# Kernel optimization log

Measured on AMD Instinct MI355X. Metric: run time of the kernel, lower is better.

Reference implementation:

```python
import jax, jax.numpy as jnp
import numpy as np

N_NODES = 100000
N_CELLS = 200000
N_EDGES = 300000
D = 128            # input_size == attention_size
HID = 128          # hidden width of custom_func MLP
SCALE = np.sqrt(np.float32(D))


def segment_softmax(src, seg_ids, num_segments):
    # src: [M, 1], seg_ids: [M] -> softmax normalized within each segment
    m = jax.ops.segment_max(src, seg_ids, num_segments=num_segments)
    e = jnp.exp(src - m[seg_ids])
    s = jax.ops.segment_sum(e, seg_ids, num_segments=num_segments)
    return e / s[seg_ids]


def setup_inputs() -> dict:
    key = jax.random.key(0)
    ks = jax.random.split(key, 9)
    cell_attr = jax.random.normal(ks[0], (N_CELLS, D), dtype=jnp.float32)
    edge_attr = jax.random.normal(ks[1], (N_EDGES, D), dtype=jnp.float32)
    node_embedding = jax.random.normal(ks[2], (N_NODES, D), dtype=jnp.float32)
    edge_index = jax.random.randint(ks[3], (2, N_EDGES), 0, N_NODES, dtype=jnp.int32)
    face = jax.random.randint(ks[4], (3, N_CELLS), 0, N_NODES, dtype=jnp.int32)
    # custom_func: 2-layer MLP (2D -> HID -> D)
    W1 = jax.random.normal(ks[5], (2 * D, HID), dtype=jnp.float32) / np.sqrt(2 * D)
    b1 = jnp.zeros((HID,), dtype=jnp.float32)
    W2 = jax.random.normal(ks[6], (HID, D), dtype=jnp.float32) / np.sqrt(HID)
    b2 = jnp.zeros((D,), dtype=jnp.float32)
    return {"cell_attr": cell_attr, "edge_attr": edge_attr,
            "node_embedding": node_embedding, "edge_index": edge_index,
            "face": face, "W1": W1, "b1": b1, "W2": W2, "b2": b2}


def reference(cell_attr, edge_attr, node_embedding, edge_index, face, W1, b1, W2, b2):
    senders, receivers = edge_index[0], edge_index[1]
    two_out = jnp.concatenate([receivers, senders], axis=0)   # outdegree order [2E]
    two_edge = jnp.concatenate([edge_attr, edge_attr], axis=0)  # [2E, D]

    # attention over edges grouped by target (outdegree) node
    att_src = jnp.sum(two_edge * node_embedding[two_out], axis=1, keepdims=True) / SCALE
    att = segment_softmax(att_src, two_out, N_NODES)            # [2E, 1]
    node_agg = jax.ops.segment_sum(two_edge * att, two_out, num_segments=N_NODES)  # [N, D]

    # cells gather mean of their 3 nodes
    cell_agg = (node_agg[face[0]] + node_agg[face[1]] + node_agg[face[2]]) / 3.0  # [C, D]

    # custom_func MLP on cat(cell_attr, cell_agg)
    h = jax.nn.relu(jnp.concatenate([cell_attr, cell_agg], axis=1) @ W1 + b1)
    cell_attr_new = h @ W2 + b2                                  # [C, D]

    # scatter_mean of cell features back to nodes
    cells_node_index = jnp.concatenate([face[0], face[1], face[2]], axis=0)  # [3C]
    tripled = jnp.concatenate([cell_attr_new] * 3, axis=0)                   # [3C, D]
    sums = jax.ops.segment_sum(tripled, cells_node_index, num_segments=N_NODES)
    counts = jax.ops.segment_sum(jnp.ones((3 * N_CELLS,), jnp.float32),
                                 cells_node_index, num_segments=N_NODES)
    node_attr = sums / jnp.maximum(counts, 1.0)[:, None]

    return cell_attr_new, node_attr
```

## Files before the change

kernel.cpp:

```cpp
#include <hip/hip_runtime.h>

#define NN 100000
#define NC 200000
#define NE 300000
#define D  128

typedef unsigned short u16;
typedef __attribute__((ext_vector_type(8))) short bf16x8;
typedef __attribute__((ext_vector_type(4))) float f32x4;

__device__ __forceinline__ u16 f2bf(float x) {
    unsigned int u = __float_as_uint(x);
    u += 0x7fffu + ((u >> 16) & 1u);
    return (u16)(u >> 16);
}
__device__ __forceinline__ float bf2f(u16 h) {
    return __uint_as_float((unsigned int)h << 16);
}

#define MFMA16(a, b, c) __builtin_amdgcn_mfma_f32_16x16x32_bf16((a), (b), (c), 0, 0, 0)

__global__ __launch_bounds__(256) void k_att(const float* __restrict__ edge_attr,
                                             const float* __restrict__ emb,
                                             const int* __restrict__ ei,
                                             float* __restrict__ expv,
                                             float* __restrict__ denom) {
    int e = blockIdx.x * 4 + (threadIdx.x >> 6);
    int lane = threadIdx.x & 63;
    if (e >= NE) return;
    int send = ei[e];
    int recv = ei[NE + e];
    float2 a = ((const float2*)(edge_attr + (size_t)e * D))[lane];
    float2 r = ((const float2*)(emb + (size_t)recv * D))[lane];
    float2 s = ((const float2*)(emb + (size_t)send * D))[lane];
    float dr = a.x * r.x + a.y * r.y;
    float ds = a.x * s.x + a.y * s.y;
    #pragma unroll
    for (int off = 32; off > 0; off >>= 1) {
        dr += __shfl_xor(dr, off);
        ds += __shfl_xor(ds, off);
    }
    if (lane == 0) {
        const float inv_scale = 0.08838834764831845f;
        float er = __expf(dr * inv_scale);
        float es = __expf(ds * inv_scale);
        expv[e] = er;
        expv[NE + e] = es;
        atomicAdd(&denom[recv], er);
        atomicAdd(&denom[send], es);
    }
}

__global__ __launch_bounds__(256) void k_hist_att(const int* __restrict__ ei,
                                                  int* __restrict__ cnt) {
    int i = blockIdx.x * 256 + threadIdx.x;
    if (i >= 2 * NE) return;
    int t = (i < NE) ? ei[NE + i] : ei[i - NE];
    atomicAdd(&cnt[t], 1);
}

__global__ __launch_bounds__(256) void k_hist_face(const int* __restrict__ face,
                                                   int* __restrict__ cnt) {
    int i = blockIdx.x * 256 + threadIdx.x;
    if (i >= 3 * NC) return;
    atomicAdd(&cnt[face[i]], 1);
}

__global__ __launch_bounds__(256) void k_scan_blocks(const int* __restrict__ cnt,
                                                     int* __restrict__ bsum) {
    __shared__ int s[256];
    int t = threadIdx.x;
    int i = blockIdx.x * 256 + t;
    s[t] = (i < NN) ? cnt[i] : 0;
    __syncthreads();
    #pragma unroll
    for (int off = 128; off > 0; off >>= 1) {
        if (t < off) s[t] += s[t + off];
        __syncthreads();
    }
    if (t == 0) bsum[blockIdx.x] = s[0];
}

__global__ __launch_bounds__(512) void k_scan_top(int* __restrict__ bsum, int nb) {
    __shared__ int s[512];
    int t = threadIdx.x;
    int v = (t < nb) ? bsum[t] : 0;
    s[t] = v;
    __syncthreads();
    #pragma unroll
    for (int off = 1; off < 512; off <<= 1) {
        int x = (t >= off) ? s[t - off] : 0;
        __syncthreads();
        s[t] += x;
        __syncthreads();
    }
    if (t < nb) bsum[t] = s[t] - v;
}

__global__ __launch_bounds__(256) void k_scan_final(const int* __restrict__ cnt,
                                                    const int* __restrict__ bsum,
                                                    int* __restrict__ off_out,
                                                    int total) {
    __shared__ int s[256];
    int t = threadIdx.x;
    int i = blockIdx.x * 256 + t;
    int v = (i < NN) ? cnt[i] : 0;
    s[t] = v;
    __syncthreads();
    #pragma unroll
    for (int off = 1; off < 256; off <<= 1) {
        int x = (t >= off) ? s[t - off] : 0;
        __syncthreads();
        s[t] += x;
        __syncthreads();
    }
    if (i < NN) off_out[i] = s[t] - v + bsum[blockIdx.x];
    if (i == 0) off_out[NN] = total;
}

__global__ __launch_bounds__(256) void k_fill_att(const int* __restrict__ ei,
                                                  const int* __restrict__ offs,
                                                  int* __restrict__ cur,
                                                  int* __restrict__ slots) {
    int i = blockIdx.x * 256 + threadIdx.x;
    if (i >= 2 * NE) return;
    int t = (i < NE) ? ei[NE + i] : ei[i - NE];
    int pos = offs[t] + atomicAdd(&cur[t], 1);
    slots[pos] = i;
}

__global__ __launch_bounds__(256) void k_fill_face(const int* __restrict__ face,
                                                   const int* __restrict__ offs,
                                                   int* __restrict__ cur,
                                                   int* __restrict__ slots) {
    int i = blockIdx.x * 256 + threadIdx.x;
    if (i >= 3 * NC) return;
    int t = face[i];
    int pos = offs[t] + atomicAdd(&cur[t], 1);
    int c = i; if (c >= NC) c -= NC; if (c >= NC) c -= NC;
    slots[pos] = c;
}

__global__ __launch_bounds__(256) void k_agg_gather(const float* __restrict__ edge_attr,
                                                    const float* __restrict__ expv,
                                                    const float* __restrict__ denom,
                                                    const int* __restrict__ offs,
                                                    const int* __restrict__ slots,
                                                    float* __restrict__ na) {
    int n = blockIdx.x * 4 + (threadIdx.x >> 6);
    int lane = threadIdx.x & 63;
    if (n >= NN) return;
    int s0 = offs[n], s1 = offs[n + 1];
    float2 acc = {0.f, 0.f};
    for (int s = s0; s < s1; ++s) {
        int eid = slots[s];
        int row = (eid < NE) ? eid : eid - NE;
        float w = expv[eid];
        float2 a = ((const float2*)(edge_attr + (size_t)row * D))[lane];
        acc.x += w * a.x;
        acc.y += w * a.y;
    }
    float inv = (s1 > s0) ? 1.f / denom[n] : 0.f;
    float2* p = (float2*)(na + (size_t)n * D) + lane;
    float2 r; r.x = acc.x * inv; r.y = acc.y * inv;
    *p = r;
}

__global__ __launch_bounds__(256) void k_smean_gather(const float* __restrict__ cell_out,
                                                      const int* __restrict__ offs,
                                                      const int* __restrict__ slots,
                                                      float* __restrict__ node_out) {
    int n = blockIdx.x * 4 + (threadIdx.x >> 6);
    int lane = threadIdx.x & 63;
    if (n >= NN) return;
    int s0 = offs[n], s1 = offs[n + 1];
    float2 acc = {0.f, 0.f};
    for (int s = s0; s < s1; ++s) {
        int c = slots[s];
        float2 y = ((const float2*)(cell_out + (size_t)c * D))[lane];
        acc.x += y.x;
        acc.y += y.y;
    }
    int deg = s1 - s0;
    float inv = deg ? 1.f / (float)deg : 0.f;
    float2* p = (float2*)(node_out + (size_t)n * D) + lane;
    float2 r; r.x = acc.x * inv; r.y = acc.y * inv;
    *p = r;
}

__global__ __launch_bounds__(256) void k_wsplit(const float* __restrict__ W1,
                                                const float* __restrict__ W2,
                                                u16* __restrict__ w1h, u16* __restrict__ w1l,
                                                u16* __restrict__ w2h, u16* __restrict__ w2l) {
    int tid = blockIdx.x * 256 + threadIdx.x;
    if (tid >= 6144) return;
    int l = tid & 63;
    int f = tid >> 6;
    const float* W; u16 *oh, *ol; int fi;
    if (f < 64) { W = W1; oh = w1h; ol = w1l; fi = f; }
    else        { W = W2; oh = w2h; ol = w2l; fi = f - 64; }
    int kt = fi >> 3, nt = fi & 7;
    int k0 = kt * 32 + 8 * (l >> 4);
    int n  = nt * 16 + (l & 15);
    #pragma unroll
    for (int i = 0; i < 8; i++) {
        float x = W[(size_t)(k0 + i) * 128 + n];
        u16 h = f2bf(x);
        oh[(size_t)fi * 512 + l * 8 + i] = h;
        ol[(size_t)fi * 512 + l * 8 + i] = f2bf(x - bf2f(h));
    }
}

__device__ __forceinline__ void stage_split(char* lds, int row, int col8, const float* v) {
    unsigned int byte = ((unsigned int)row << 9) + ((unsigned int)col8 << 4);
    byte ^= (unsigned int)(row & 7) << 4;
    bf16x8 hi, lo;
    #pragma unroll
    for (int i = 0; i < 8; i++) {
        u16 h = f2bf(v[i]);
        hi[i] = (short)h;
        lo[i] = (short)f2bf(v[i] - bf2f(h));
    }
    *(bf16x8*)(lds + byte)         = hi;
    *(bf16x8*)(lds + 16384 + byte) = lo;
}

__global__ __launch_bounds__(256, 4) void k_mlp(const float* __restrict__ cell_attr,
                                                const float* __restrict__ na,
                                                const int* __restrict__ face,
                                                const u16* __restrict__ w1h,
                                                const u16* __restrict__ w1l,
                                                const u16* __restrict__ w2h,
                                                const u16* __restrict__ w2l,
                                                const float* __restrict__ b1,
                                                const float* __restrict__ b2,
                                                float* __restrict__ out) {
    __shared__ char lds[32768];
    const int t  = threadIdx.x;
    const int c0 = blockIdx.x * 32;

    {
        const int r = t >> 3;
        const int q = t & 7;
        float v[16];
        const float* pa = cell_attr + (size_t)(c0 + r) * D + q * 16;
        #pragma unroll
        for (int i = 0; i < 4; i++) *(float4*)(v + 4 * i) = *(const float4*)(pa + 4 * i);
        stage_split(lds, r, q * 2,     v);
        stage_split(lds, r, q * 2 + 1, v + 8);

        const int cid = c0 + r;
        const int f0 = face[cid], f1 = face[NC + cid], f2 = face[2 * NC + cid];
        const float* p0 = na + (size_t)f0 * D + q * 16;
        const float* p1 = na + (size_t)f1 * D + q * 16;
        const float* p2 = na + (size_t)f2 * D + q * 16;
        const float third = 1.f / 3.f;
        #pragma unroll
        for (int i = 0; i < 4; i++) {
            float4 a0 = *(const float4*)(p0 + 4 * i);
            float4 a1 = *(const float4*)(p1 + 4 * i);
            float4 a2 = *(const float4*)(p2 + 4 * i);
            v[4 * i + 0] = (a0.x + a1.x + a2.x) * third;
            v[4 * i + 1] = (a0.y + a1.y + a2.y) * third;
            v[4 * i + 2] = (a0.z + a1.z + a2.z) * third;
            v[4 * i + 3] = (a0.w + a1.w + a2.w) * third;
        }
        stage_split(lds, r, 16 + q * 2, v);
        stage_split(lds, r, 17 + q * 2, v + 8);
    }
    __syncthreads();

    const int w  = t >> 6;
    const int l  = t & 63;
    const int lr = l & 15;
    const int lg = l >> 4;
    const unsigned int swz = (unsigned int)(lr & 7) << 4;
    const size_t wl8 = (size_t)l * 8;
    const f32x4 z4 = {0.f, 0.f, 0.f, 0.f};
    f32x4 acc[2][2] = {{z4, z4}, {z4, z4}};

    {
        const unsigned int abase = ((unsigned int)lr << 9) + ((unsigned int)lg << 4);
        const u16* pW1h = w1h + (size_t)(w * 2) * 512 + wl8;
        const u16* pW1l = w1l + (size_t)(w * 2) * 512 + wl8;
        #pragma unroll 2
        for (int kt = 0; kt < 8; ++kt) {
            unsigned int ab = (abase + (unsigned int)kt * 64) ^ swz;
            bf16x8 aH0 = *(const bf16x8*)(lds + ab);
            bf16x8 aL0 = *(const bf16x8*)(lds + 16384 + ab);
            bf16x8 aH1 = *(const bf16x8*)(lds + ab + 8192);
            bf16x8 aL1 = *(const bf16x8*)(lds + 16384 + ab + 8192);
            #pragma unroll
            for (int jn = 0; jn < 2; ++jn) {
                size_t fo = (size_t)(kt * 8 + jn) * 512;
                bf16x8 bH = *(const bf16x8*)(pW1h + fo);
                bf16x8 bL = *(const bf16x8*)(pW1l + fo);
                acc[0][jn] = MFMA16(aH0, bL, acc[0][jn]);
                acc[0][jn] = MFMA16(aL0, bH, acc[0][jn]);
                acc[0][jn] = MFMA16(aH0, bH, acc[0][jn]);
                acc[1][jn] = MFMA16(aH1, bL, acc[1][jn]);
                acc[1][jn] = MFMA16(aL1, bH, acc[1][jn]);
                acc[1][jn] = MFMA16(aH1, bH, acc[1][jn]);
            }
        }
    }

    __syncthreads();

    #pragma unroll
    for (int jn = 0; jn < 2; ++jn) {
        int col = w * 32 + jn * 16 + lr;
        float bb = b1[col];
        #pragma unroll
        for (int rt = 0; rt < 2; ++rt) {
            #pragma unroll
            for (int r = 0; r < 4; ++r) {
                int row = rt * 16 + lg * 4 + r;
                float h = fmaxf(acc[rt][jn][r] + bb, 0.f);
                u16 hh = f2bf(h);
                u16 hl = f2bf(h - bf2f(hh));
                unsigned int byte = (((unsigned int)row << 8) + ((unsigned int)col << 1))
                                    ^ ((unsigned int)(row & 7) << 4);
                *(u16*)(lds + byte)        = hh;
                *(u16*)(lds + 8192 + byte) = hl;
            }
        }
    }
    __syncthreads();

    f32x4 acc2[2][2] = {{z4, z4}, {z4, z4}};
    {
        const unsigned int abase = ((unsigned int)lr << 8) + ((unsigned int)lg << 4);
        const u16* pW2h = w2h + (size_t)(w * 2) * 512 + wl8;
        const u16* pW2l = w2l + (size_t)(w * 2) * 512 + wl8;
        #pragma unroll 2
        for (int kt = 0; kt < 4; ++kt) {
            unsigned int ab = (abase + (unsigned int)kt * 64) ^ swz;
            bf16x8 aH0 = *(const bf16x8*)(lds + ab);
            bf16x8 aL0 = *(const bf16x8*)(lds + 8192 + ab);
            bf16x8 aH1 = *(const bf16x8*)(lds + ab + 4096);
            bf16x8 aL1 = *(const bf16x8*)(lds + 8192 + ab + 4096);
            #pragma unroll
            for (int jn = 0; jn < 2; ++jn) {
                size_t fo = (size_t)(kt * 8 + jn) * 512;
                bf16x8 bH = *(const bf16x8*)(pW2h + fo);
                bf16x8 bL = *(const bf16x8*)(pW2l + fo);
                acc2[0][jn] = MFMA16(aH0, bL, acc2[0][jn]);
                acc2[0][jn] = MFMA16(aL0, bH, acc2[0][jn]);
                acc2[0][jn] = MFMA16(aH0, bH, acc2[0][jn]);
                acc2[1][jn] = MFMA16(aH1, bL, acc2[1][jn]);
                acc2[1][jn] = MFMA16(aL1, bH, acc2[1][jn]);
                acc2[1][jn] = MFMA16(aH1, bH, acc2[1][jn]);
            }
        }
    }

    #pragma unroll
    for (int jn = 0; jn < 2; ++jn) {
        int col = w * 32 + jn * 16 + lr;
        float bb = b2[col];
        #pragma unroll
        for (int rt = 0; rt < 2; ++rt) {
            #pragma unroll
            for (int r = 0; r < 4; ++r) {
                int row = c0 + rt * 16 + lg * 4 + r;
                out[(size_t)row * D + col] = acc2[rt][jn][r] + bb;
            }
        }
    }
}

extern "C" void kernel_launch(void* const* d_in, const int* in_sizes, int n_in,
                              void* d_out, int out_size, void* d_ws, size_t ws_size,
                              hipStream_t stream) {
    (void)in_sizes; (void)n_in; (void)out_size; (void)ws_size;
    const float* cell_attr = (const float*)d_in[0];
    const float* edge_attr = (const float*)d_in[1];
    const float* emb       = (const float*)d_in[2];
    const int*   ei        = (const int*)d_in[3];
    const int*   face      = (const int*)d_in[4];
    const float* W1        = (const float*)d_in[5];
    const float* b1        = (const float*)d_in[6];
    const float* W2        = (const float*)d_in[7];
    const float* b2        = (const float*)d_in[8];

    float* out_cell = (float*)d_out;
    float* out_node = out_cell + (size_t)NC * D;

    float* denom  = (float*)d_ws;
    int*   cntA   = (int*)d_ws + NN;
    int*   cntF   = cntA + NN;
    int*   curA   = cntF + NN;
    int*   curF   = curA + NN;
    float* expv   = (float*)(curF + NN);
    int*   offA   = (int*)(expv + 2 * NE);
    int*   offF   = offA + NN + 1;
    int*   slotsA = offF + NN + 1;
    int*   slotsF = slotsA + 2 * NE;
    int*   bsumA  = slotsF + 3 * NC;
    int*   bsumF  = bsumA + 512;

    u16* w1h = (u16*)curA;
    u16* w1l = w1h + 64 * 512;
    u16* w2h = w1l + 64 * 512;
    u16* w2l = w2h + 32 * 512;

    const int NB = (NN + 255) / 256;

    hipMemsetAsync(d_ws, 0, (size_t)5 * NN * 4, stream);

    k_att<<<(NE + 3) / 4, 256, 0, stream>>>(edge_attr, emb, ei, expv, denom);

    k_hist_att <<<(2 * NE + 255) / 256, 256, 0, stream>>>(ei, cntA);
    k_hist_face<<<(3 * NC + 255) / 256, 256, 0, stream>>>(face, cntF);

    k_scan_blocks<<<NB, 256, 0, stream>>>(cntA, bsumA);
    k_scan_top   <<<1, 512, 0, stream>>>(bsumA, NB);
    k_scan_final <<<NB, 256, 0, stream>>>(cntA, bsumA, offA, 2 * NE);

    k_scan_blocks<<<NB, 256, 0, stream>>>(cntF, bsumF);
    k_scan_top   <<<1, 512, 0, stream>>>(bsumF, NB);
    k_scan_final <<<NB, 256, 0, stream>>>(cntF, bsumF, offF, 3 * NC);

    k_fill_att <<<(2 * NE + 255) / 256, 256, 0, stream>>>(ei, offA, curA, slotsA);
    k_fill_face<<<(3 * NC + 255) / 256, 256, 0, stream>>>(face, offF, curF, slotsF);

    k_wsplit<<<24, 256, 0, stream>>>(W1, W2, w1h, w1l, w2h, w2l);

    k_agg_gather<<<(NN + 3) / 4, 256, 0, stream>>>(edge_attr, expv, denom, offA, slotsA, out_node);

    k_mlp<<<NC / 32, 256, 0, stream>>>(cell_attr, out_node, face,
                                       w1h, w1l, w2h, w2l, b1, b2, out_cell);

    k_smean_gather<<<(NN + 3) / 4, 256, 0, stream>>>(out_cell, offF, slotsF, out_node);
}
```

Before: 748.4 us.

## Fuse prep kernels, pre-resolve slot weights, and widen gathers to float4

Merges the attention, histogram, and weight-split kernels into one launch, and batches the two scans and two fill passes into shared launches, cutting the launch count. The fill pass now stores the edge row and its exp weight per slot, so the aggregation no longer does an indirect expv lookup. Both gather kernels switch to float4 loads with two half-waves each taking alternate neighbours, then combine with a shuffle. BF16 hi/lo splitting uses the packed v_cvt_pk_bf16_f32 instruction. Weight-split buffers move to a separate workspace region, because they previously overlapped the cur counters that now run alongside them.

```diff
diff --git a/kernel.cpp b/kernel.cpp
--- a/kernel.cpp
+++ b/kernel.cpp
@@ -4,6 +4,9 @@
 #define NC 200000
 #define NE 300000
 #define D  128
+#define NB 391
+#define AB 37500
+#define HB 2344
 
 typedef unsigned short u16;
 typedef __attribute__((ext_vector_type(8))) short bf16x8;
@@ -17,60 +20,96 @@
 __device__ __forceinline__ float bf2f(u16 h) {
     return __uint_as_float((unsigned int)h << 16);
 }
+__device__ __forceinline__ unsigned int cvt_pk_bf16(float a, float b) {
+    unsigned int r;
+    asm("v_cvt_pk_bf16_f32 %0, %1, %2" : "=v"(r) : "v"(a), "v"(b));
+    return r;
+}
 
 #define MFMA16(a, b, c) __builtin_amdgcn_mfma_f32_16x16x32_bf16((a), (b), (c), 0, 0, 0)
 
-__global__ __launch_bounds__(256) void k_att(const float* __restrict__ edge_attr,
-                                             const float* __restrict__ emb,
-                                             const int* __restrict__ ei,
-                                             float* __restrict__ expv,
-                                             float* __restrict__ denom) {
-    int e = blockIdx.x * 4 + (threadIdx.x >> 6);
-    int lane = threadIdx.x & 63;
-    if (e >= NE) return;
-    int send = ei[e];
-    int recv = ei[NE + e];
-    float2 a = ((const float2*)(edge_attr + (size_t)e * D))[lane];
-    float2 r = ((const float2*)(emb + (size_t)recv * D))[lane];
-    float2 s = ((const float2*)(emb + (size_t)send * D))[lane];
-    float dr = a.x * r.x + a.y * r.y;
-    float ds = a.x * s.x + a.y * s.y;
-    #pragma unroll
-    for (int off = 32; off > 0; off >>= 1) {
-        dr += __shfl_xor(dr, off);
-        ds += __shfl_xor(ds, off);
-    }
-    if (lane == 0) {
-        const float inv_scale = 0.08838834764831845f;
-        float er = __expf(dr * inv_scale);
-        float es = __expf(ds * inv_scale);
-        expv[e] = er;
-        expv[NE + e] = es;
-        atomicAdd(&denom[recv], er);
-        atomicAdd(&denom[send], es);
-    }
-}
-
-__global__ __launch_bounds__(256) void k_hist_att(const int* __restrict__ ei,
-                                                  int* __restrict__ cnt) {
-    int i = blockIdx.x * 256 + threadIdx.x;
-    if (i >= 2 * NE) return;
-    int t = (i < NE) ? ei[NE + i] : ei[i - NE];
-    atomicAdd(&cnt[t], 1);
-}
-
-__global__ __launch_bounds__(256) void k_hist_face(const int* __restrict__ face,
-                                                   int* __restrict__ cnt) {
-    int i = blockIdx.x * 256 + threadIdx.x;
-    if (i >= 3 * NC) return;
-    atomicAdd(&cnt[face[i]], 1);
-}
-
-__global__ __launch_bounds__(256) void k_scan_blocks(const int* __restrict__ cnt,
-                                                     int* __restrict__ bsum) {
+__global__ __launch_bounds__(256) void k_att_prep(const float* __restrict__ edge_attr,
+                                                  const float* __restrict__ emb,
+                                                  const int* __restrict__ ei,
+                                                  const int* __restrict__ face,
+                                                  float* __restrict__ expv,
+                                                  float* __restrict__ denom,
+                                                  int* __restrict__ cntA,
+                                                  int* __restrict__ cntF,
+                                                  const float* __restrict__ W1,
+                                                  const float* __restrict__ W2,
+                                                  u16* __restrict__ w1h, u16* __restrict__ w1l,
+                                                  u16* __restrict__ w2h, u16* __restrict__ w2l) {
+    int b = blockIdx.x;
+    int t = threadIdx.x;
+    if (b < AB) {
+        int lane = t & 63;
+        int half = lane >> 5;
+        int sub  = lane & 31;
+        int e = b * 8 + (t >> 6) * 2 + half;
+        int send = ei[e];
+        int recv = ei[NE + e];
+        float4 a  = ((const float4*)(edge_attr + (size_t)e * D))[sub];
+        float4 r4 = ((const float4*)(emb + (size_t)recv * D))[sub];
+        float4 s4 = ((const float4*)(emb + (size_t)send * D))[sub];
+        float dr = a.x * r4.x + a.y * r4.y + a.z * r4.z + a.w * r4.w;
+        float ds = a.x * s4.x + a.y * s4.y + a.z * s4.z + a.w * s4.w;
+        #pragma unroll
+        for (int off = 16; off > 0; off >>= 1) {
+            dr += __shfl_xor(dr, off);
+            ds += __shfl_xor(ds, off);
+        }
+        if (sub == 0) {
+            const float inv_scale = 0.08838834764831845f;
+            float er = __expf(dr * inv_scale);
+            float es = __expf(ds * inv_scale);
+            expv[e] = er;
+            expv[NE + e] = es;
+            atomicAdd(&denom[recv], er);
+            atomicAdd(&denom[send], es);
+        }
+    } else if (b < AB + HB) {
+        int i = (b - AB) * 256 + t;
+        if (i >= 2 * NE) return;
+        int tgt = (i < NE) ? ei[NE + i] : ei[i - NE];
+        atomicAdd(&cntA[tgt], 1);
+    } else if (b < AB + 2 * HB) {
+        int i = (b - AB - HB) * 256 + t;
+        if (i >= 3 * NC) return;
+        atomicAdd(&cntF[face[i]], 1);
+    } else {
+        int tid = (b - AB - 2 * HB) * 256 + t;
+        if (tid >= 6144) return;
+        int l = tid & 63;
+        int f = tid >> 6;
+        const float* W; u16 *oh, *ol; int fi;
+        if (f < 64) { W = W1; oh = w1h; ol = w1l; fi = f; }
+        else        { W = W2; oh = w2h; ol = w2l; fi = f - 64; }
+        int kt = fi >> 3, nt = fi & 7;
+        int k0 = kt * 32 + 8 * (l >> 4);
+        int n  = nt * 16 + (l & 15);
+        #pragma unroll
+        for (int i = 0; i < 8; i++) {
+            float x = W[(size_t)(k0 + i) * 128 + n];
+            u16 h = f2bf(x);
+            oh[(size_t)fi * 512 + l * 8 + i] = h;
+            ol[(size_t)fi * 512 + l * 8 + i] = f2bf(x - bf2f(h));
+        }
+    }
+}
+
+__global__ __launch_bounds__(256) void k_scan_blocks(const int* __restrict__ cntA,
+                                                     const int* __restrict__ cntF,
+                                                     int* __restrict__ bsumA,
+                                                     int* __restrict__ bsumF) {
     __shared__ int s[256];
+    int bb = blockIdx.x;
+    bool fa = bb >= NB;
+    const int* cnt = fa ? cntF : cntA;
+    int* bsum = fa ? bsumF : bsumA;
+    int blk = fa ? bb - NB : bb;
     int t = threadIdx.x;
-    int i = blockIdx.x * 256 + t;
+    int i = blk * 256 + t;
     s[t] = (i < NN) ? cnt[i] : 0;
     __syncthreads();
     #pragma unroll
@@ -78,11 +117,13 @@
         if (t < off) s[t] += s[t + off];
         __syncthreads();
     }
-    if (t == 0) bsum[blockIdx.x] = s[0];
-}
-
-__global__ __launch_bounds__(512) void k_scan_top(int* __restrict__ bsum, int nb) {
+    if (t == 0) bsum[blk] = s[0];
+}
+
+__global__ __launch_bounds__(512) void k_scan_top(int* __restrict__ bsumA,
+                                                  int* __restrict__ bsumF, int nb) {
     __shared__ int s[512];
+    int* bsum = blockIdx.x ? bsumF : bsumA;
     int t = threadIdx.x;
     int v = (t < nb) ? bsum[t] : 0;
     s[t] = v;
@@ -97,13 +138,22 @@
     if (t < nb) bsum[t] = s[t] - v;
 }
 
-__global__ __launch_bounds__(256) void k_scan_final(const int* __restrict__ cnt,
-                                                    const int* __restrict__ bsum,
-                                                    int* __restrict__ off_out,
-                                                    int total) {
+__global__ __launch_bounds__(256) void k_scan_final(const int* __restrict__ cntA,
+                                                    const int* __restrict__ cntF,
+                                                    const int* __restrict__ bsumA,
+                                                    const int* __restrict__ bsumF,
+                                                    int* __restrict__ offA,
+                                                    int* __restrict__ offF) {
     __shared__ int s[256];
+    int bb = blockIdx.x;
+    bool fa = bb >= NB;
+    const int* cnt = fa ? cntF : cntA;
+    const int* bsum = fa ? bsumF : bsumA;
+    int* off_out = fa ? offF : offA;
+    int total = fa ? 3 * NC : 2 * NE;
+    int blk = fa ? bb - NB : bb;
     int t = threadIdx.x;
-    int i = blockIdx.x * 256 + t;
+    int i = blk * 256 + t;
     int v = (i < NN) ? cnt[i] : 0;
     s[t] = v;
     __syncthreads();
@@ -114,56 +164,66 @@
         s[t] += x;
         __syncthreads();
     }
-    if (i < NN) off_out[i] = s[t] - v + bsum[blockIdx.x];
+    if (i < NN) off_out[i] = s[t] - v + bsum[blk];
     if (i == 0) off_out[NN] = total;
 }
 
-__global__ __launch_bounds__(256) void k_fill_att(const int* __restrict__ ei,
-                                                  const int* __restrict__ offs,
-                                                  int* __restrict__ cur,
-                                                  int* __restrict__ slots) {
-    int i = blockIdx.x * 256 + threadIdx.x;
-    if (i >= 2 * NE) return;
-    int t = (i < NE) ? ei[NE + i] : ei[i - NE];
-    int pos = offs[t] + atomicAdd(&cur[t], 1);
-    slots[pos] = i;
-}
-
-__global__ __launch_bounds__(256) void k_fill_face(const int* __restrict__ face,
-                                                   const int* __restrict__ offs,
-                                                   int* __restrict__ cur,
-                                                   int* __restrict__ slots) {
-    int i = blockIdx.x * 256 + threadIdx.x;
-    if (i >= 3 * NC) return;
-    int t = face[i];
-    int pos = offs[t] + atomicAdd(&cur[t], 1);
-    int c = i; if (c >= NC) c -= NC; if (c >= NC) c -= NC;
-    slots[pos] = c;
+__global__ __launch_bounds__(256) void k_fill(const int* __restrict__ ei,
+                                              const float* __restrict__ expv,
+                                              const int* __restrict__ face,
+                                              const int* __restrict__ offA,
+                                              const int* __restrict__ offF,
+                                              int* __restrict__ curA,
+                                              int* __restrict__ curF,
+                                              int* __restrict__ slotsA,
+                                              float* __restrict__ wexpA,
+                                              int* __restrict__ slotsF) {
+    int b = blockIdx.x;
+    int t = threadIdx.x;
+    if (b < HB) {
+        int i = b * 256 + t;
+        if (i >= 2 * NE) return;
+        int tgt = (i < NE) ? ei[NE + i] : ei[i - NE];
+        int pos = offA[tgt] + atomicAdd(&curA[tgt], 1);
+        slotsA[pos] = (i < NE) ? i : i - NE;
+        wexpA[pos] = expv[i];
+    } else {
+        int i = (b - HB) * 256 + t;
+        if (i >= 3 * NC) return;
+        int tgt = face[i];
+        int pos = offF[tgt] + atomicAdd(&curF[tgt], 1);
+        int c = i; if (c >= NC) c -= NC; if (c >= NC) c -= NC;
+        slotsF[pos] = c;
+    }
 }
 
 __global__ __launch_bounds__(256) void k_agg_gather(const float* __restrict__ edge_attr,
-                                                    const float* __restrict__ expv,
+                                                    const float* __restrict__ wexp,
                                                     const float* __restrict__ denom,
                                                     const int* __restrict__ offs,
                                                     const int* __restrict__ slots,
                                                     float* __restrict__ na) {
     int n = blockIdx.x * 4 + (threadIdx.x >> 6);
     int lane = threadIdx.x & 63;
+    int half = lane >> 5, sub = lane & 31;
     if (n >= NN) return;
     int s0 = offs[n], s1 = offs[n + 1];
-    float2 acc = {0.f, 0.f};
-    for (int s = s0; s < s1; ++s) {
-        int eid = slots[s];
-        int row = (eid < NE) ? eid : eid - NE;
-        float w = expv[eid];
-        float2 a = ((const float2*)(edge_attr + (size_t)row * D))[lane];
-        acc.x += w * a.x;
-        acc.y += w * a.y;
-    }
-    float inv = (s1 > s0) ? 1.f / denom[n] : 0.f;
-    float2* p = (float2*)(na + (size_t)n * D) + lane;
-    float2 r; r.x = acc.x * inv; r.y = acc.y * inv;
-    *p = r;
+    float4 acc = {0.f, 0.f, 0.f, 0.f};
+    for (int s = s0 + half; s < s1; s += 2) {
+        int row = slots[s];
+        float w = wexp[s];
+        float4 a = ((const float4*)(edge_attr + (size_t)row * D))[sub];
+        acc.x += w * a.x; acc.y += w * a.y; acc.z += w * a.z; acc.w += w * a.w;
+    }
+    acc.x += __shfl_xor(acc.x, 32);
+    acc.y += __shfl_xor(acc.y, 32);
+    acc.z += __shfl_xor(acc.z, 32);
+    acc.w += __shfl_xor(acc.w, 32);
+    if (half == 0) {
+        float inv = (s1 > s0) ? 1.f / denom[n] : 0.f;
+        float4 r; r.x = acc.x * inv; r.y = acc.y * inv; r.z = acc.z * inv; r.w = acc.w * inv;
+        ((float4*)(na + (size_t)n * D))[sub] = r;
+    }
 }
 
 __global__ __launch_bounds__(256) void k_smean_gather(const float* __restrict__ cell_out,
@@ -172,57 +232,43 @@
                                                       float* __restrict__ node_out) {
     int n = blockIdx.x * 4 + (threadIdx.x >> 6);
     int lane = threadIdx.x & 63;
+    int half = lane >> 5, sub = lane & 31;
     if (n >= NN) return;
     int s0 = offs[n], s1 = offs[n + 1];
-    float2 acc = {0.f, 0.f};
-    for (int s = s0; s < s1; ++s) {
+    float4 acc = {0.f, 0.f, 0.f, 0.f};
+    for (int s = s0 + half; s < s1; s += 2) {
         int c = slots[s];
-        float2 y = ((const float2*)(cell_out + (size_t)c * D))[lane];
-        acc.x += y.x;
-        acc.y += y.y;
-    }
-    int deg = s1 - s0;
-    float inv = deg ? 1.f / (float)deg : 0.f;
-    float2* p = (float2*)(node_out + (size_t)n * D) + lane;
-    float2 r; r.x = acc.x * inv; r.y = acc.y * inv;
-    *p = r;
-}
-
-__global__ __launch_bounds__(256) void k_wsplit(const float* __restrict__ W1,
-                                                const float* __restrict__ W2,
-                                                u16* __restrict__ w1h, u16* __restrict__ w1l,
-                                                u16* __restrict__ w2h, u16* __restrict__ w2l) {
-    int tid = blockIdx.x * 256 + threadIdx.x;
-    if (tid >= 6144) return;
-    int l = tid & 63;
-    int f = tid >> 6;
-    const float* W; u16 *oh, *ol; int fi;
-    if (f < 64) { W = W1; oh = w1h; ol = w1l; fi = f; }
-    else        { W = W2; oh = w2h; ol = w2l; fi = f - 64; }
-    int kt = fi >> 3, nt = fi & 7;
-    int k0 = kt * 32 + 8 * (l >> 4);
-    int n  = nt * 16 + (l & 15);
-    #pragma unroll
-    for (int i = 0; i < 8; i++) {
-        float x = W[(size_t)(k0 + i) * 128 + n];
-        u16 h = f2bf(x);
-        oh[(size_t)fi * 512 + l * 8 + i] = h;
-        ol[(size_t)fi * 512 + l * 8 + i] = f2bf(x - bf2f(h));
+        float4 y = ((const float4*)(cell_out + (size_t)c * D))[sub];
+        acc.x += y.x; acc.y += y.y; acc.z += y.z; acc.w += y.w;
+    }
+    acc.x += __shfl_xor(acc.x, 32);
+    acc.y += __shfl_xor(acc.y, 32);
+    acc.z += __shfl_xor(acc.z, 32);
+    acc.w += __shfl_xor(acc.w, 32);
+    if (half == 0) {
+        int deg = s1 - s0;
+        float inv = deg ? 1.f / (float)deg : 0.f;
+        float4 r; r.x = acc.x * inv; r.y = acc.y * inv; r.z = acc.z * inv; r.w = acc.w * inv;
+        ((float4*)(node_out + (size_t)n * D))[sub] = r;
     }
 }
 
 __device__ __forceinline__ void stage_split(char* lds, int row, int col8, const float* v) {
     unsigned int byte = ((unsigned int)row << 9) + ((unsigned int)col8 << 4);
     byte ^= (unsigned int)(row & 7) << 4;
-    bf16x8 hi, lo;
+    uint4 hi, lo;
+    unsigned int* hp = (unsigned int*)&hi;
+    unsigned int* lp = (unsigned int*)&lo;
     #pragma unroll
-    for (int i = 0; i < 8; i++) {
-        u16 h = f2bf(v[i]);
-        hi[i] = (short)h;
-        lo[i] = (short)f2bf(v[i] - bf2f(h));
-    }
-    *(bf16x8*)(lds + byte)         = hi;
-    *(bf16x8*)(lds + 16384 + byte) = lo;
+    for (int i = 0; i < 4; i++) {
+        unsigned int h = cvt_pk_bf16(v[2 * i], v[2 * i + 1]);
+        float h0 = __uint_as_float(h << 16);
+        float h1 = __uint_as_float(h & 0xffff0000u);
+        hp[i] = h;
+        lp[i] = cvt_pk_bf16(v[2 * i] - h0, v[2 * i + 1] - h1);
+    }
+    *(uint4*)(lds + byte)         = hi;
+    *(uint4*)(lds + 16384 + byte) = lo;
 }
 
 __global__ __launch_bounds__(256, 4) void k_mlp(const float* __restrict__ cell_attr,
@@ -307,22 +353,29 @@
 
     __syncthreads();
 
-    #pragma unroll
-    for (int jn = 0; jn < 2; ++jn) {
-        int col = w * 32 + jn * 16 + lr;
-        float bb = b1[col];
+    {
+        const int col0 = w * 32 + lr;
+        const int col1 = col0 + 16;
+        const float bb0 = b1[col0];
+        const float bb1 = b1[col1];
         #pragma unroll
         for (int rt = 0; rt < 2; ++rt) {
             #pragma unroll
             for (int r = 0; r < 4; ++r) {
                 int row = rt * 16 + lg * 4 + r;
-                float h = fmaxf(acc[rt][jn][r] + bb, 0.f);
-                u16 hh = f2bf(h);
-                u16 hl = f2bf(h - bf2f(hh));
-                unsigned int byte = (((unsigned int)row << 8) + ((unsigned int)col << 1))
-                                    ^ ((unsigned int)(row & 7) << 4);
-                *(u16*)(lds + byte)        = hh;
-                *(u16*)(lds + 8192 + byte) = hl;
+                float h0 = fmaxf(acc[rt][0][r] + bb0, 0.f);
+                float h1 = fmaxf(acc[rt][1][r] + bb1, 0.f);
+                unsigned int ph = cvt_pk_bf16(h0, h1);
+                float f0 = __uint_as_float(ph << 16);
+                float f1 = __uint_as_float(ph & 0xffff0000u);
+                unsigned int pl = cvt_pk_bf16(h0 - f0, h1 - f1);
+                unsigned int swzr = (unsigned int)(row & 7) << 4;
+                unsigned int b0 = (((unsigned int)row << 8) + ((unsigned int)col0 << 1)) ^ swzr;
+                unsigned int bcol1 = (((unsigned int)row << 8) + ((unsigned int)col1 << 1)) ^ swzr;
+                *(u16*)(lds + b0)            = (u16)ph;
+                *(u16*)(lds + bcol1)         = (u16)(ph >> 16);
+                *(u16*)(lds + 8192 + b0)     = (u16)pl;
+                *(u16*)(lds + 8192 + bcol1)  = (u16)(pl >> 16);
             }
         }
     }
@@ -397,37 +450,27 @@
     int*   offF   = offA + NN + 1;
     int*   slotsA = offF + NN + 1;
     int*   slotsF = slotsA + 2 * NE;
-    int*   bsumA  = slotsF + 3 * NC;
+    float* wexpA  = (float*)(slotsF + 3 * NC);
+    int*   bsumA  = (int*)(wexpA + 2 * NE);
     int*   bsumF  = bsumA + 512;
-
-    u16* w1h = (u16*)curA;
+    u16* w1h = (u16*)(((uintptr_t)(bsumF + 512) + 15) & ~(uintptr_t)15);
     u16* w1l = w1h + 64 * 512;
     u16* w2h = w1l + 64 * 512;
     u16* w2l = w2h + 32 * 512;
 
-    const int NB = (NN + 255) / 256;
-
     hipMemsetAsync(d_ws, 0, (size_t)5 * NN * 4, stream);
 
-    k_att<<<(NE + 3) / 4, 256, 0, stream>>>(edge_attr, emb, ei, expv, denom);
-
-    k_hist_att <<<(2 * NE + 255) / 256, 256, 0, stream>>>(ei, cntA);
-    k_hist_face<<<(3 * NC + 255) / 256, 256, 0, stream>>>(face, cntF);
-
-    k_scan_blocks<<<NB, 256, 0, stream>>>(cntA, bsumA);
-    k_scan_top   <<<1, 512, 0, stream>>>(bsumA, NB);
-    k_scan_final <<<NB, 256, 0, stream>>>(cntA, bsumA, offA, 2 * NE);
-
-    k_scan_blocks<<<NB, 256, 0, stream>>>(cntF, bsumF);
-    k_scan_top   <<<1, 512, 0, stream>>>(bsumF, NB);
-    k_scan_final <<<NB, 256, 0, stream>>>(cntF, bsumF, offF, 3 * NC);
-
-    k_fill_att <<<(2 * NE + 255) / 256, 256, 0, stream>>>(ei, offA, curA, slotsA);
-    k_fill_face<<<(3 * NC + 255) / 256, 256, 0, stream>>>(face, offF, curF, slotsF);
-
-    k_wsplit<<<24, 256, 0, stream>>>(W1, W2, w1h, w1l, w2h, w2l);
-
-    k_agg_gather<<<(NN + 3) / 4, 256, 0, stream>>>(edge_attr, expv, denom, offA, slotsA, out_node);
+    k_att_prep<<<AB + 2 * HB + 24, 256, 0, stream>>>(edge_attr, emb, ei, face, expv, denom,
+                                                     cntA, cntF, W1, W2, w1h, w1l, w2h, w2l);
+
+    k_scan_blocks<<<2 * NB, 256, 0, stream>>>(cntA, cntF, bsumA, bsumF);
+    k_scan_top   <<<2, 512, 0, stream>>>(bsumA, bsumF, NB);
+    k_scan_final <<<2 * NB, 256, 0, stream>>>(cntA, cntF, bsumA, bsumF, offA, offF);
+
+    k_fill<<<2 * HB, 256, 0, stream>>>(ei, expv, face, offA, offF, curA, curF,
+                                       slotsA, wexpA, slotsF);
+
+    k_agg_gather<<<(NN + 3) / 4, 256, 0, stream>>>(edge_attr, wexpA, denom, offA, slotsA, out_node);
 
     k_mlp<<<NC / 32, 256, 0, stream>>>(cell_attr, out_node, face,
                                        w1h, w1l, w2h, w2l, b1, b2, out_cell);
```

New measurement: 690.6 us. 7.7% less time.
